# Performance work log

Hardware: AMD Instinct MI355X
Metric: run time of the kernel (lower is better)

## Reference

```python
import jax, jax.numpy as jnp
import numpy as np

G = 4      # groups (conv groups == offset groups)
KS = 3     # kernel size
DIL = 1    # dilation
PAD = 1    # padding = dilation
EPS = 1e-5 # InstanceNorm eps


def setup_inputs() -> dict:
    key = jax.random.key(0)
    k1, k2, k3, k4, k5 = jax.random.split(key, 5)
    B, C, D, H, W = 4, 64, 8, 64, 64
    Cout = 64
    Cg = C // G
    x = jax.random.normal(k1, (B, C, D, H, W), jnp.float32)
    # small offset-conv weights so predicted offsets stay within a few pixels
    w_off = jax.random.normal(k2, (2 * KS * KS * G, Cg, KS, KS), jnp.float32) * 0.01
    b_off = jax.random.normal(k3, (2 * KS * KS * G,), jnp.float32) * 0.01
    w_dc = jax.random.normal(k4, (Cout, Cg, KS, KS), jnp.float32) * (1.0 / np.sqrt(Cg * KS * KS))
    b_dc = jax.random.normal(k5, (Cout,), jnp.float32) * 0.01
    return {"x": x, "w_off": w_off, "b_off": b_off, "w_dc": w_dc, "b_dc": b_dc}


def reference(x, w_off, b_off, w_dc, b_dc):
    B, C, D, H, W = x.shape
    N = B * D
    K = KS * KS
    Cg = C // G
    # torch .view(B*D, C, H, W) is a row-major reshape of the flat buffer
    x2 = x.reshape(N, C, H, W)

    # grouped 3x3 offset conv, same padding
    off = jax.lax.conv_general_dilated(
        x2, w_off, (1, 1), [(PAD, PAD), (PAD, PAD)],
        rhs_dilation=(DIL, DIL), feature_group_count=G,
        dimension_numbers=("NCHW", "OIHW", "NCHW"),
    ) + b_off[None, :, None, None]
    off = off.reshape(N, G, K, 2, H, W)        # (y, x) offset per group/kernel-pt
    dy, dx = off[:, :, :, 0], off[:, :, :, 1]  # [N,G,K,H,W]

    # base sampling grid per kernel point
    ki, kj = jnp.meshgrid(jnp.arange(KS), jnp.arange(KS), indexing="ij")
    ki = ki.reshape(K); kj = kj.reshape(K)
    base_y = (jnp.arange(H)[None, :] - PAD + ki[:, None] * DIL).astype(jnp.float32)  # [K,H]
    base_x = (jnp.arange(W)[None, :] - PAD + kj[:, None] * DIL).astype(jnp.float32)  # [K,W]
    py = base_y[None, None, :, :, None] + dy   # [N,G,K,H,W]
    px = base_x[None, None, :, None, :] + dx

    y0 = jnp.floor(py); x0 = jnp.floor(px)
    ly = py - y0; lx = px - x0
    y0i = y0.astype(jnp.int32); x0i = x0.astype(jnp.int32)

    xg = x2.reshape(N, G, Cg, H * W)
    gather = jax.vmap(jax.vmap(lambda xf, idx: xf[:, idx]))  # over N, G

    def corner(yi, xi, w):
        valid = (yi >= 0) & (yi < H) & (xi >= 0) & (xi < W)   # zero-pad OOB
        idx = jnp.clip(yi, 0, H - 1) * W + jnp.clip(xi, 0, W - 1)
        v = gather(xg, idx.reshape(N, G, -1)).reshape(N, G, Cg, K, H, W)
        return v * (w * valid)[:, :, None]                    # broadcast over Cg

    val = (corner(y0i,     x0i,     (1 - ly) * (1 - lx))
         + corner(y0i,     x0i + 1, (1 - ly) * lx)
         + corner(y0i + 1, x0i,     ly * (1 - lx))
         + corner(y0i + 1, x0i + 1, ly * lx))                 # [N,G,Cg,K,H,W]

    wg = w_dc.reshape(G, -1, Cg, K)                           # [G,Coutg,Cg,K]
    out = jnp.einsum("gock,ngckhw->ngohw", wg, val).reshape(N, -1, H, W)
    out = out + b_dc[None, :, None, None]

    # InstanceNorm2d (affine=False, biased var) + exact GELU
    m = out.mean((-2, -1), keepdims=True)
    v = out.var((-2, -1), keepdims=True)
    out = jax.nn.gelu((out - m) * jax.lax.rsqrt(v + EPS), approximate=False)

    Cout = out.shape[1]
    return out.reshape(B, D, Cout, H, W).transpose(0, 2, 1, 3, 4)  # [B,Cout,D,H,W]
```

## Files before the change

### kernel.cpp

```cpp
#include <hip/hip_runtime.h>
#include <hip/hip_bf16.h>
#include <math.h>

#define HW 4096
#define NN 32
#define W68 68
#define SLICE (68 * 68)

typedef __attribute__((ext_vector_type(8))) short bf16x8;
typedef __attribute__((ext_vector_type(4))) float f32x4;

__device__ inline unsigned short bfbits(float a) {
    __hip_bfloat16 h = __float2bfloat16(a);
    unsigned short u;
    __builtin_memcpy(&u, &h, 2);
    return u;
}
__device__ inline unsigned packbf(float a, float b) {
    return (unsigned)bfbits(a) | ((unsigned)bfbits(b) << 16);
}
__device__ inline float bflo(unsigned u) { return __uint_as_float(u << 16); }
__device__ inline float bfhi(unsigned u) { return __uint_as_float(u & 0xffff0000u); }

__device__ inline void bilin8(uint4 A, uint4 B, uint4 C, uint4 D,
                              const float* ww, float* val) {
    const unsigned* ua = (const unsigned*)&A;
    const unsigned* ub = (const unsigned*)&B;
    const unsigned* uc = (const unsigned*)&C;
    const unsigned* ud = (const unsigned*)&D;
    #pragma unroll
    for (int j = 0; j < 4; j++) {
        val[2*j]   = ww[0]*bflo(ua[j]) + ww[1]*bflo(ub[j]) + ww[2]*bflo(uc[j]) + ww[3]*bflo(ud[j]);
        val[2*j+1] = ww[0]*bfhi(ua[j]) + ww[1]*bfhi(ub[j]) + ww[2]*bfhi(uc[j]) + ww[3]*bfhi(ud[j]);
    }
}

__global__ __launch_bounds__(256) void transpose_x(const float* __restrict__ x,
                                                   unsigned short* __restrict__ xT,
                                                   const float* __restrict__ w_off,
                                                   const float* __restrict__ w_dc,
                                                   unsigned short* __restrict__ wperm)
{
    int bx = blockIdx.x;
    int t = threadIdx.x;

    if (bx < 120) {
        int idx = bx * 256 + t;
        int g = idx / 7680;
        int r3 = idx - g * 7680;
        int which = r3 / 2560;
        int r = r3 - which * 2560;
        int j = r & 7;
        int rest = r >> 3;
        int nn_ = rest & 15; rest >>= 4;
        int q_ = rest & 3, kp_ = rest >> 2;
        int k = q_ * 8 + j;
        int c = k & 15, tt = kp_ * 2 + (k >> 4);
        float v = 0.f;
        if (tt < 9) {
            if (which == 0)      v = w_dc[(g * 16 + nn_) * 144 + c * 9 + tt];
            else if (which == 1) v = w_off[(g * 18 + nn_) * 144 + c * 9 + tt];
            else if (nn_ < 2)    v = w_off[(g * 18 + 16 + nn_) * 144 + c * 9 + tt];
        }
        wperm[idx] = bfbits(v);
    }

    __shared__ float tile[256 * 17];
    int n = bx >> 6, g = (bx >> 4) & 3, chunk = bx & 15;
    const float* xb = x + (size_t)(n * 64 + g * 16) * HW + chunk * 256;

    #pragma unroll
    for (int r = 0; r < 16; r++) {
        int idx = r * 256 + t;
        int c = idx >> 8, p = idx & 255;
        tile[p * 17 + c] = xb[c * HW + p];
    }
    __syncthreads();

    unsigned short* ob = xT + (size_t)(n * 4 + g) * SLICE * 16;
    #pragma unroll
    for (int r = 0; r < 2; r++) {
        int idx = r * 256 + t;
        int p = idx >> 1, half = idx & 1;
        int pos = chunk * 256 + p;
        int h = pos >> 6, w = pos & 63;
        const float* tp = &tile[p * 17 + half * 8];
        uint4 v;
        v.x = packbf(tp[0], tp[1]);
        v.y = packbf(tp[2], tp[3]);
        v.z = packbf(tp[4], tp[5]);
        v.w = packbf(tp[6], tp[7]);
        *(uint4*)(ob + ((size_t)((h + 2) * W68 + (w + 2)) * 16 + half * 8)) = v;
    }
}

__global__ __launch_bounds__(256) void fused_conv(const unsigned short* __restrict__ xT,
                                                  const unsigned short* __restrict__ wperm,
                                                  const float* __restrict__ b_off,
                                                  const float* __restrict__ b_dc,
                                                  float* __restrict__ outpre)
{
    __shared__ __attribute__((aligned(16))) unsigned short wfrag[7680];
    __shared__ __attribute__((aligned(4)))  unsigned short off_lds[256 * 20];

    int bx = blockIdx.x;
    int n = bx >> 6, g = (bx >> 4) & 3, chunk = bx & 15;
    int t = threadIdx.x;
    int lane = t & 63, wv = t >> 6;
    int nn = lane & 15, q = lane >> 4;
    int t2 = q >> 1, chh = q & 1;

    {
        const uint4* src = (const uint4*)(wperm + g * 7680);
        uint4* dst = (uint4*)wfrag;
        #pragma unroll
        for (int r = 0; r < 4; r++) {
            int idx = r * 256 + t;
            if (idx < 960) dst[idx] = src[idx];
        }
    }
    __syncthreads();

    const unsigned short* xw = xT + (size_t)(n * 4 + g) * SLICE * 16 + chh * 8;

    {
        f32x4 acc0[4], acc1[4];
        float bv0 = b_off[g * 18 + nn];
        float bv1 = (nn < 2) ? b_off[g * 18 + 16 + nn] : 0.f;
        #pragma unroll
        for (int s = 0; s < 4; s++)
            #pragma unroll
            for (int r = 0; r < 4; r++) { acc0[s][r] = bv0; acc1[s][r] = bv1; }

        #pragma unroll
        for (int kp = 0; kp < 5; kp++) {
            int fo = ((kp * 4 + q) * 16 + nn) * 8;
            bf16x8 b0 = *(const bf16x8*)&wfrag[2560 + fo];
            bf16x8 b1 = *(const bf16x8*)&wfrag[5120 + fo];
            int tap = kp * 2 + t2;
            int ki = tap / 3, kj = tap - ki * 3;
            #pragma unroll
            for (int s = 0; s < 4; s++) {
                int pos = chunk * 256 + (wv * 4 + s) * 16 + nn;
                int h = pos >> 6, w = pos & 63;
                int base = (h + 1 + ki) * W68 + (w + 1 + kj);
                uint4 v = *(const uint4*)(xw + (size_t)base * 16);
                bf16x8 af = *(bf16x8*)&v;
                acc0[s] = __builtin_amdgcn_mfma_f32_16x16x32_bf16(af, b0, acc0[s], 0, 0, 0);
                acc1[s] = __builtin_amdgcn_mfma_f32_16x16x32_bf16(af, b1, acc1[s], 0, 0, 0);
            }
        }

        #pragma unroll
        for (int s = 0; s < 4; s++) {
            int pl = (wv * 4 + s) * 16 + q * 4;
            #pragma unroll
            for (int r = 0; r < 4; r++) {
                off_lds[(pl + r) * 20 + nn] = bfbits(acc0[s][r]);
                if (nn < 2)
                    off_lds[(pl + r) * 20 + 16 + nn] = bfbits(acc1[s][r]);
            }
        }
    }
    __syncthreads();

    f32x4 acc[4];
    float bv = b_dc[g * 16 + nn];
    #pragma unroll
    for (int s = 0; s < 4; s++)
        #pragma unroll
        for (int r = 0; r < 4; r++) acc[s][r] = bv;

    #pragma unroll
    for (int kp = 0; kp < 5; kp++) {
        bf16x8 bw = *(const bf16x8*)&wfrag[((kp * 4 + q) * 16 + nn) * 8];
        int tap = kp * 2 + t2;
        int ki = tap / 3, kj = tap - ki * 3;
        #pragma unroll
        for (int s = 0; s < 4; s++) {
            int pl = (wv * 4 + s) * 16 + nn;
            int pos = chunk * 256 + pl;
            int h = pos >> 6, w = pos & 63;
            bf16x8 af = {0, 0, 0, 0, 0, 0, 0, 0};
            if (tap < 9) {
                unsigned u = *(const unsigned*)&off_lds[pl * 20 + 2 * tap];
                float py = (float)(h - 1 + ki) + bflo(u);
                float px = (float)(w - 1 + kj) + bfhi(u);
                float y0f = fminf(fmaxf(floorf(py), -2.f), 64.f);
                float x0f = fminf(fmaxf(floorf(px), -2.f), 64.f);
                float ly = py - y0f, lx = px - x0f;
                float my = 1.f - ly, mx = 1.f - lx;
                float ww[4] = { my * mx, my * lx, ly * mx, ly * lx };
                int y0 = (int)y0f, x0 = (int)x0f;
                int base = (y0 + 2) * W68 + (x0 + 2);
                const unsigned short* p0 = xw + (size_t)base * 16;
                uint4 A = *(const uint4*)(p0);
                uint4 B = *(const uint4*)(p0 + 16);
                uint4 C = *(const uint4*)(p0 + W68 * 16);
                uint4 D = *(const uint4*)(p0 + W68 * 16 + 16);
                float val[8];
                bilin8(A, B, C, D, ww, val);
                #pragma unroll
                for (int j = 0; j < 8; j++) af[j] = (short)bfbits(val[j]);
            }
            acc[s] = __builtin_amdgcn_mfma_f32_16x16x32_bf16(af, bw, acc[s], 0, 0, 0);
        }
    }

    float* op = outpre + (size_t)(n * 64 + g * 16) * HW;
    #pragma unroll
    for (int s = 0; s < 4; s++) {
        int pbase = chunk * 256 + (wv * 4 + s) * 16 + q * 4;
        #pragma unroll
        for (int r = 0; r < 4; r++)
            op[nn * HW + pbase + r] = acc[s][r];
    }
}

__global__ __launch_bounds__(256) void norm_gelu(const float* __restrict__ outpre,
                                                 float* __restrict__ out)
{
    __shared__ float red[8];
    int bx = blockIdx.x;
    int n  = bx >> 6;
    int co = bx & 63;
    int t  = threadIdx.x;

    const float4* base = (const float4*)(outpre + (size_t)(n * 64 + co) * HW);
    float4 v[4];
    float s = 0.f, sq = 0.f;
    #pragma unroll
    for (int r = 0; r < 4; r++) {
        v[r] = base[t + r * 256];
        s  += v[r].x + v[r].y + v[r].z + v[r].w;
        sq  = fmaf(v[r].x, v[r].x, sq);
        sq  = fmaf(v[r].y, v[r].y, sq);
        sq  = fmaf(v[r].z, v[r].z, sq);
        sq  = fmaf(v[r].w, v[r].w, sq);
    }
    #pragma unroll
    for (int o2 = 32; o2 > 0; o2 >>= 1) {
        s  += __shfl_down(s,  o2, 64);
        sq += __shfl_down(sq, o2, 64);
    }
    int wid = t >> 6, lane = t & 63;
    if (lane == 0) { red[wid] = s; red[4 + wid] = sq; }
    __syncthreads();
    float S  = red[0] + red[1] + red[2] + red[3];
    float SQ = red[4] + red[5] + red[6] + red[7];
    float mean = S * (1.f / 4096.f);
    float var  = SQ * (1.f / 4096.f) - mean * mean;
    float rstd = rsqrtf(var + 1e-5f);

    int b = n >> 3, d = n & 7;
    float4* outp = (float4*)(out + ((size_t)(b * 64 + co) * 8 + d) * HW);
    #pragma unroll
    for (int r = 0; r < 4; r++) {
        float xs[4] = {v[r].x, v[r].y, v[r].z, v[r].w};
        float4 res;
        float* rp = (float*)&res;
        #pragma unroll
        for (int qq = 0; qq < 4; qq++) {
            float xn = (xs[qq] - mean) * rstd;
            float u = xn * (1.5957691f + 0.0713548162f * xn * xn);
            float e = __expf(-u);
            rp[qq] = xn * __frcp_rn(1.f + e);
        }
        outp[t + r * 256] = res;
    }
}

extern "C" void kernel_launch(void* const* d_in, const int* in_sizes, int n_in,
                              void* d_out, int out_size, void* d_ws, size_t ws_size,
                              hipStream_t stream) {
    const float* x     = (const float*)d_in[0];
    const float* w_off = (const float*)d_in[1];
    const float* b_off = (const float*)d_in[2];  (void)b_off;
    const float* w_dc  = (const float*)d_in[3];
    const float* b_dc  = (const float*)d_in[4];
    float* out = (float*)d_out;

    unsigned short* wperm = (unsigned short*)d_ws;
    unsigned short* xTb   = wperm + 30720;
    float* outpre = (float*)(xTb + (size_t)NN * 4 * SLICE * 16);

    hipMemsetAsync(d_ws, 0, 61440 + (size_t)NN * 4 * SLICE * 16 * 2, stream);

    transpose_x<<<2048, 256, 0, stream>>>(x, xTb, w_off, w_dc, wperm);
    fused_conv <<<2048, 256, 0, stream>>>(xTb, wperm,
                                          (const float*)d_in[2], b_dc, outpre);
    norm_gelu  <<<2048, 256, 0, stream>>>(outpre, out);
}
```

Measured before the change: 148.2 us.

## Keep conv weights in registers and software-pipeline gathers in fused_conv

Weight fragments are loaded straight from global memory into registers instead of being staged through LDS, which drops one barrier and the LDS weight array. Both the offset-conv loop and the deformable-sampling loop now use double-buffered register prefetch. The next tap's gather loads are issued before the current MFMA, so memory latency overlaps with compute. The padded tenth tap no longer uses a branch: its offsets are zero-filled and its weights are expected to be zero. The kernel also gets a launch_bounds occupancy hint of 4. The costs are higher register pressure and reads past the slice for the padded tap, which could touch memory beyond the last slice.

```diff
diff --git a/kernel.cpp b/kernel.cpp
--- a/kernel.cpp
+++ b/kernel.cpp
@@ -94,14 +94,13 @@
     }
 }
 
-__global__ __launch_bounds__(256) void fused_conv(const unsigned short* __restrict__ xT,
-                                                  const unsigned short* __restrict__ wperm,
-                                                  const float* __restrict__ b_off,
-                                                  const float* __restrict__ b_dc,
-                                                  float* __restrict__ outpre)
+__global__ __launch_bounds__(256, 4) void fused_conv(const unsigned short* __restrict__ xT,
+                                                     const unsigned short* __restrict__ wperm,
+                                                     const float* __restrict__ b_off,
+                                                     const float* __restrict__ b_dc,
+                                                     float* __restrict__ outpre)
 {
-    __shared__ __attribute__((aligned(16))) unsigned short wfrag[7680];
-    __shared__ __attribute__((aligned(4)))  unsigned short off_lds[256 * 20];
+    __shared__ __attribute__((aligned(8))) unsigned short off_lds[256 * 20];
 
     int bx = blockIdx.x;
     int n = bx >> 6, g = (bx >> 4) & 3, chunk = bx & 15;
@@ -110,20 +109,30 @@
     int nn = lane & 15, q = lane >> 4;
     int t2 = q >> 1, chh = q & 1;
 
+    const unsigned short* wpg = wperm + g * 7680;
+    const unsigned short* xw = xT + (size_t)(n * 4 + g) * SLICE * 16 + chh * 8;
+
+    int pls[4]; float fy[4], fx[4]; int basep[4];
+    #pragma unroll
+    for (int s = 0; s < 4; s++) {
+        int pl = (wv * 4 + s) * 16 + nn;
+        int pos = chunk * 256 + pl;
+        int h = pos >> 6, w = pos & 63;
+        pls[s] = pl;
+        fy[s] = (float)(h - 1);
+        fx[s] = (float)(w - 1);
+        basep[s] = (h + 1) * W68 + (w + 1);
+    }
+
     {
-        const uint4* src = (const uint4*)(wperm + g * 7680);
-        uint4* dst = (uint4*)wfrag;
-        #pragma unroll
-        for (int r = 0; r < 4; r++) {
-            int idx = r * 256 + t;
-            if (idx < 960) dst[idx] = src[idx];
-        }
-    }
-    __syncthreads();
-
-    const unsigned short* xw = xT + (size_t)(n * 4 + g) * SLICE * 16 + chh * 8;
-
-    {
+        bf16x8 pb0[5], pb1[5];
+        #pragma unroll
+        for (int kp = 0; kp < 5; kp++) {
+            int fo = ((kp * 4 + q) * 16 + nn) * 8;
+            pb0[kp] = *(const bf16x8*)(wpg + 2560 + fo);
+            pb1[kp] = *(const bf16x8*)(wpg + 5120 + fo);
+        }
+
         f32x4 acc0[4], acc1[4];
         float bv0 = b_off[g * 18 + nn];
         float bv1 = (nn < 2) ? b_off[g * 18 + 16 + nn] : 0.f;
@@ -132,22 +141,26 @@
             #pragma unroll
             for (int r = 0; r < 4; r++) { acc0[s][r] = bv0; acc1[s][r] = bv1; }
 
+        uint4 xv[2][4];
+        auto stage1 = [&](int kp) {
+            int ki = t2 ? (2 * kp + 1) / 3 : (2 * kp) / 3;
+            int kj = t2 ? (2 * kp + 1) % 3 : (2 * kp) % 3;
+            int xo = ki * W68 + kj;
+            int sl = kp & 1;
+            #pragma unroll
+            for (int s = 0; s < 4; s++)
+                xv[sl][s] = *(const uint4*)(xw + (size_t)(basep[s] + xo) * 16);
+        };
+        stage1(0);
         #pragma unroll
         for (int kp = 0; kp < 5; kp++) {
-            int fo = ((kp * 4 + q) * 16 + nn) * 8;
-            bf16x8 b0 = *(const bf16x8*)&wfrag[2560 + fo];
-            bf16x8 b1 = *(const bf16x8*)&wfrag[5120 + fo];
-            int tap = kp * 2 + t2;
-            int ki = tap / 3, kj = tap - ki * 3;
+            if (kp < 4) stage1(kp + 1);
+            int sl = kp & 1;
             #pragma unroll
             for (int s = 0; s < 4; s++) {
-                int pos = chunk * 256 + (wv * 4 + s) * 16 + nn;
-                int h = pos >> 6, w = pos & 63;
-                int base = (h + 1 + ki) * W68 + (w + 1 + kj);
-                uint4 v = *(const uint4*)(xw + (size_t)base * 16);
-                bf16x8 af = *(bf16x8*)&v;
-                acc0[s] = __builtin_amdgcn_mfma_f32_16x16x32_bf16(af, b0, acc0[s], 0, 0, 0);
-                acc1[s] = __builtin_amdgcn_mfma_f32_16x16x32_bf16(af, b1, acc1[s], 0, 0, 0);
+                bf16x8 af = *(bf16x8*)&xv[sl][s];
+                acc0[s] = __builtin_amdgcn_mfma_f32_16x16x32_bf16(af, pb0[kp], acc0[s], 0, 0, 0);
+                acc1[s] = __builtin_amdgcn_mfma_f32_16x16x32_bf16(af, pb1[kp], acc1[s], 0, 0, 0);
             }
         }
 
@@ -161,7 +174,15 @@
                     off_lds[(pl + r) * 20 + 16 + nn] = bfbits(acc1[s][r]);
             }
         }
-    }
+        off_lds[t * 20 + 18] = 0;
+        off_lds[t * 20 + 19] = 0;
+    }
+
+    bf16x8 bwr[5];
+    #pragma unroll
+    for (int kp = 0; kp < 5; kp++)
+        bwr[kp] = *(const bf16x8*)(wpg + ((kp * 4 + q) * 16 + nn) * 8);
+
     __syncthreads();
 
     f32x4 acc[4];
@@ -171,40 +192,45 @@
         #pragma unroll
         for (int r = 0; r < 4; r++) acc[s][r] = bv;
 
-    #pragma unroll
-    for (int kp = 0; kp < 5; kp++) {
-        bf16x8 bw = *(const bf16x8*)&wfrag[((kp * 4 + q) * 16 + nn) * 8];
-        int tap = kp * 2 + t2;
-        int ki = tap / 3, kj = tap - ki * 3;
-        #pragma unroll
-        for (int s = 0; s < 4; s++) {
-            int pl = (wv * 4 + s) * 16 + nn;
-            int pos = chunk * 256 + pl;
-            int h = pos >> 6, w = pos & 63;
-            bf16x8 af = {0, 0, 0, 0, 0, 0, 0, 0};
-            if (tap < 9) {
-                unsigned u = *(const unsigned*)&off_lds[pl * 20 + 2 * tap];
-                float py = (float)(h - 1 + ki) + bflo(u);
-                float px = (float)(w - 1 + kj) + bfhi(u);
-                float y0f = fminf(fmaxf(floorf(py), -2.f), 64.f);
-                float x0f = fminf(fmaxf(floorf(px), -2.f), 64.f);
-                float ly = py - y0f, lx = px - x0f;
-                float my = 1.f - ly, mx = 1.f - lx;
-                float ww[4] = { my * mx, my * lx, ly * mx, ly * lx };
-                int y0 = (int)y0f, x0 = (int)x0f;
-                int base = (y0 + 2) * W68 + (x0 + 2);
-                const unsigned short* p0 = xw + (size_t)base * 16;
-                uint4 A = *(const uint4*)(p0);
-                uint4 B = *(const uint4*)(p0 + 16);
-                uint4 C = *(const uint4*)(p0 + W68 * 16);
-                uint4 D = *(const uint4*)(p0 + W68 * 16 + 16);
-                float val[8];
-                bilin8(A, B, C, D, ww, val);
-                #pragma unroll
-                for (int j = 0; j < 8; j++) af[j] = (short)bfbits(val[j]);
-            }
-            acc[s] = __builtin_amdgcn_mfma_f32_16x16x32_bf16(af, bw, acc[s], 0, 0, 0);
-        }
+    uint4 RA[2], RB[2], RC[2], RD[2];
+    float rw[2][4];
+
+    auto stage = [&](int u) {
+        int kp = u >> 2, s = u & 3, sl = u & 1;
+        int ki = t2 ? (2 * kp + 1) / 3 : (2 * kp) / 3;
+        int kj = t2 ? (2 * kp + 1) % 3 : (2 * kp) % 3;
+        int tap2 = 4 * kp + 2 * t2;
+        unsigned uo = *(const unsigned*)&off_lds[pls[s] * 20 + tap2];
+        float py = fy[s] + (float)ki + bflo(uo);
+        float px = fx[s] + (float)kj + bfhi(uo);
+        float y0f = fminf(fmaxf(floorf(py), -2.f), 64.f);
+        float x0f = fminf(fmaxf(floorf(px), -2.f), 64.f);
+        float ly = py - y0f, lx = px - x0f;
+        float my = 1.f - ly, mx = 1.f - lx;
+        rw[sl][0] = my * mx; rw[sl][1] = my * lx;
+        rw[sl][2] = ly * mx; rw[sl][3] = ly * lx;
+        int base = (int)(y0f * 68.f + x0f) + 138;
+        const unsigned short* p0 = xw + (size_t)base * 16;
+        RA[sl] = *(const uint4*)(p0);
+        RB[sl] = *(const uint4*)(p0 + 16);
+        RC[sl] = *(const uint4*)(p0 + W68 * 16);
+        RD[sl] = *(const uint4*)(p0 + W68 * 16 + 16);
+    };
+    auto consume = [&](int u) {
+        int kp = u >> 2, s = u & 3, sl = u & 1;
+        float val[8];
+        bilin8(RA[sl], RB[sl], RC[sl], RD[sl], rw[sl], val);
+        bf16x8 af;
+        #pragma unroll
+        for (int j = 0; j < 8; j++) af[j] = (short)bfbits(val[j]);
+        acc[s] = __builtin_amdgcn_mfma_f32_16x16x32_bf16(af, bwr[kp], acc[s], 0, 0, 0);
+    };
+
+    stage(0);
+    #pragma unroll
+    for (int u = 0; u < 20; u++) {
+        if (u < 19) stage(u + 1);
+        consume(u);
     }
 
     float* op = outpre + (size_t)(n * 64 + g * 16) * HW;
```

After: 145.7 us. Within noise of the previous version (-1.7%).
